# Performance work log

Hardware: AMD Instinct MI355X
Metric: run time of the kernel (lower is better)

## Reference

```python
import jax, jax.numpy as jnp
import numpy as np

ALPHA_F = 0.1
ALPHA_L = 1.0
ALPHA_E = 1.0
V_E = 10.0


def _conv3(y, w):
    # torch Conv1d(1,1,3,padding=1), cross-correlation with 3-tap kernel w
    yp = jnp.pad(y, ((0, 0), (1, 1)))  # [B, L+2]
    return w[0] * yp[:, :-2] + w[1] * yp[:, 1:-1] + w[2] * yp[:, 2:]


def setup_inputs() -> dict:
    key = jax.random.key(0)
    k1, k2 = jax.random.split(key)
    B, T, L = 32, 64, 8192
    x = jax.random.normal(k1, (B, T, L), dtype=jnp.float32)
    w = jax.random.normal(k2, (3,), dtype=jnp.float32) * 0.1  # learned Conv1d kernel
    return {"x": x, "w": w}


def reference(x, w):
    # x: [B, T, L]; PCNN recurrence over T steps
    B, T, L = x.shape
    df = jnp.asarray(np.exp(-ALPHA_F), dtype=x.dtype)
    dl = jnp.asarray(np.exp(-ALPHA_L), dtype=x.dtype)
    de = jnp.asarray(np.exp(-ALPHA_E), dtype=x.dtype)

    def step(carry, x_n):
        f, l, e, y = carry
        f = df * f + x_n + _conv3(y, w)
        # settled_weight=True: fixed kernel [1, 0, 1]
        yp = jnp.pad(y, ((0, 0), (1, 1)))
        l = dl * l + yp[:, :-2] + yp[:, 2:]
        u = f * (1.0 + 0.5 * l)
        e = de * e + V_E * y
        y = jax.nn.sigmoid(u - e)
        return (f, l, e, y), y

    z = jnp.zeros((B, L), dtype=x.dtype)
    e0 = jnp.full((B, L), V_E / ALPHA_E, dtype=x.dtype)
    _, ys = jax.lax.scan(step, (z, z, e0, z), jnp.swapaxes(x, 0, 1))  # ys: [T, B, L]
    return jnp.swapaxes(ys, 0, 1)  # [B, T, L]
```

## Files before the change

kernel.cpp:

```cpp
#include <hip/hip_runtime.h>
#include <hip/hip_bf16.h>

#define BB 32
#define TT 64
#define LL 8192
#define CC 512
#define HH 64
#define RR (CC + 2 * HH)
#define NTHREADS (RR / 2)
#define NCHUNK (LL / CC)

__device__ __forceinline__ float fsigmoid(float z) {
    float ex = __expf(-z);
    return __fdividef(1.0f, 1.0f + ex);
}

__global__ __launch_bounds__(NTHREADS) void pcnn_kernel(
    const float* __restrict__ x, const float* __restrict__ wptr,
    float* __restrict__ out)
{
    __shared__ float ylds[2 * RR];

    const int tid   = threadIdx.x;
    const int blk   = blockIdx.x;
    const int chunk = blk & (NCHUNK - 1);
    const int b     = blk >> 4;

    const float w0 = wptr[0], w1 = wptr[1], w2 = wptr[2];
    const float df = 0.90483741803595957f;
    const float dl = 0.36787944117144233f;
    const float de = 0.36787944117144233f;

    const int r0 = 2 * tid;
    const int g0 = chunk * CC - HH + r0;
    const bool valid = (g0 >= 0) && (g0 < LL);
    const bool store_en = (r0 >= HH) && (r0 < HH + CC);

    ylds[r0] = 0.0f; ylds[r0 + 1] = 0.0f;
    ylds[RR + r0] = 0.0f; ylds[RR + r0 + 1] = 0.0f;
    __syncthreads();

    float f0 = 0.f, f1 = 0.f, l0 = 0.f, l1 = 0.f;
    float e0 = 10.f, e1 = 10.f, y0 = 0.f, y1 = 0.f;

    const float* xrow = x + (size_t)b * TT * LL;
    float*       orow = out + (size_t)b * TT * LL;

    float2 xc = valid ? *(const float2*)(xrow + g0) : make_float2(0.f, 0.f);

    int cur = 0;
    for (int t = 0; t < TT; ++t) {
        float2 xn = make_float2(0.f, 0.f);
        if ((t + 1 < TT) && valid)
            xn = *(const float2*)(xrow + (size_t)(t + 1) * LL + g0);

        float yl = (r0 == 0)       ? 0.f : ylds[cur * RR + r0 - 1];
        float yr = (r0 + 2 >= RR)  ? 0.f : ylds[cur * RR + r0 + 2];

        f0 = df * f0 + xc.x + (w0 * yl + w1 * y0 + w2 * y1);
        f1 = df * f1 + xc.y + (w0 * y0 + w1 * y1 + w2 * yr);
        l0 = dl * l0 + yl + y1;
        l1 = dl * l1 + y0 + yr;
        float u0 = f0 * (1.0f + 0.5f * l0);
        float u1 = f1 * (1.0f + 0.5f * l1);
        e0 = de * e0 + 10.0f * y0;
        e1 = de * e1 + 10.0f * y1;

        float ny0 = valid ? fsigmoid(u0 - e0) : 0.f;
        float ny1 = valid ? fsigmoid(u1 - e1) : 0.f;
        y0 = ny0; y1 = ny1;

        const int nxt = cur ^ 1;
        *(float2*)&ylds[nxt * RR + r0] = make_float2(y0, y1);

        if (store_en)
            *(float2*)(orow + (size_t)t * LL + g0) = make_float2(y0, y1);

        __syncthreads();
        cur = nxt;
        xc = xn;
    }
}

extern "C" void kernel_launch(void* const* d_in, const int* in_sizes, int n_in,
                              void* d_out, int out_size, void* d_ws, size_t ws_size,
                              hipStream_t stream) {
    const float* x = (const float*)d_in[0];
    const float* w = (const float*)d_in[1];
    float* out = (float*)d_out;
    pcnn_kernel<<<dim3(BB * NCHUNK), dim3(NTHREADS), 0, stream>>>(x, w, out);
}
```

Baseline: 158.1 us.

## Map each tile to one wavefront, exchanging halos via shuffles instead of LDS barriers

Each 640-column tile (512 output plus 64-column halos) is now handled by a single 64-lane wavefront, with five float2 elements per lane held in registers. Neighbour values move through cross-lane shuffles, so the shared-memory ping-pong buffer and the per-step __syncthreads are gone. The x loads are double-buffered two time steps ahead to hide global latency. The cost is fewer threads in total (512 wavefronts in 256 blocks of 128), more registers per lane, and more serial work per lane.

```diff
diff --git a/kernel.cpp b/kernel.cpp
--- a/kernel.cpp
+++ b/kernel.cpp
@@ -1,84 +1,110 @@
 #include <hip/hip_runtime.h>
 #include <hip/hip_bf16.h>
 
-#define BB 32
+
 #define TT 64
 #define LL 8192
 #define CC 512
 #define HH 64
-#define RR (CC + 2 * HH)
-#define NTHREADS (RR / 2)
-#define NCHUNK (LL / CC)
+#define RR 640
+#define KS 5
+#define NCHUNK 16
 
 __device__ __forceinline__ float fsigmoid(float z) {
     float ex = __expf(-z);
     return __fdividef(1.0f, 1.0f + ex);
 }
 
-__global__ __launch_bounds__(NTHREADS) void pcnn_kernel(
+__global__ __launch_bounds__(128) void pcnn_wave_kernel(
     const float* __restrict__ x, const float* __restrict__ wptr,
     float* __restrict__ out)
 {
-    __shared__ float ylds[2 * RR];
-
-    const int tid   = threadIdx.x;
-    const int blk   = blockIdx.x;
-    const int chunk = blk & (NCHUNK - 1);
-    const int b     = blk >> 4;
+    const int lane = threadIdx.x & 63;
+    const int tile = blockIdx.x * 2 + (threadIdx.x >> 6);
+    const int chunk = tile & (NCHUNK - 1);
+    const int b     = tile >> 4;
 
     const float w0 = wptr[0], w1 = wptr[1], w2 = wptr[2];
     const float df = 0.90483741803595957f;
     const float dl = 0.36787944117144233f;
     const float de = 0.36787944117144233f;
 
-    const int r0 = 2 * tid;
-    const int g0 = chunk * CC - HH + r0;
-    const bool valid = (g0 >= 0) && (g0 < LL);
-    const bool store_en = (r0 >= HH) && (r0 < HH + CC);
+    const int gbase = chunk * CC - HH;
 
-    ylds[r0] = 0.0f; ylds[r0 + 1] = 0.0f;
-    ylds[RR + r0] = 0.0f; ylds[RR + r0 + 1] = 0.0f;
-    __syncthreads();
-
-    float f0 = 0.f, f1 = 0.f, l0 = 0.f, l1 = 0.f;
-    float e0 = 10.f, e1 = 10.f, y0 = 0.f, y1 = 0.f;
+    int  col[KS];
+    bool vz[KS];
+    bool st[KS];
+    #pragma unroll
+    for (int k = 0; k < KS; ++k) {
+        const int r = 128 * k + 2 * lane;
+        col[k] = gbase + r;
+        vz[k]  = (col[k] >= 0) && (col[k] < LL);
+        st[k]  = (r >= HH) && (r < HH + CC);
+    }
 
     const float* xrow = x + (size_t)b * TT * LL;
     float*       orow = out + (size_t)b * TT * LL;
 
-    float2 xc = valid ? *(const float2*)(xrow + g0) : make_float2(0.f, 0.f);
+    float2 xb[2][KS];
+    #pragma unroll
+    for (int k = 0; k < KS; ++k)
+        xb[0][k] = vz[k] ? *(const float2*)(xrow + col[k]) : make_float2(0.f, 0.f);
+    #pragma unroll
+    for (int k = 0; k < KS; ++k)
+        xb[1][k] = vz[k] ? *(const float2*)(xrow + LL + col[k]) : make_float2(0.f, 0.f);
 
-    int cur = 0;
+    float2 f[KS], l[KS], e[KS], y[KS];
+    #pragma unroll
+    for (int k = 0; k < KS; ++k) {
+        f[k] = make_float2(0.f, 0.f);
+        l[k] = make_float2(0.f, 0.f);
+        e[k] = make_float2(10.f, 10.f);
+        y[k] = make_float2(0.f, 0.f);
+    }
+
     for (int t = 0; t < TT; ++t) {
-        float2 xn = make_float2(0.f, 0.f);
-        if ((t + 1 < TT) && valid)
-            xn = *(const float2*)(xrow + (size_t)(t + 1) * LL + g0);
+        const int cur = t & 1;
+        float2 xc[KS];
+        #pragma unroll
+        for (int k = 0; k < KS; ++k) xc[k] = xb[cur][k];
 
-        float yl = (r0 == 0)       ? 0.f : ylds[cur * RR + r0 - 1];
-        float yr = (r0 + 2 >= RR)  ? 0.f : ylds[cur * RR + r0 + 2];
+        if (t + 2 < TT) {
+            const float* xnxt = xrow + (size_t)(t + 2) * LL;
+            #pragma unroll
+            for (int k = 0; k < KS; ++k)
+                xb[cur][k] = vz[k] ? *(const float2*)(xnxt + col[k]) : make_float2(0.f, 0.f);
+        }
 
-        f0 = df * f0 + xc.x + (w0 * yl + w1 * y0 + w2 * y1);
-        f1 = df * f1 + xc.y + (w0 * y0 + w1 * y1 + w2 * yr);
-        l0 = dl * l0 + yl + y1;
-        l1 = dl * l1 + y0 + yr;
-        float u0 = f0 * (1.0f + 0.5f * l0);
-        float u1 = f1 * (1.0f + 0.5f * l1);
-        e0 = de * e0 + 10.0f * y0;
-        e1 = de * e1 + 10.0f * y1;
+        float rl[KS], rr[KS], yl[KS], yr[KS];
+        #pragma unroll
+        for (int k = 0; k < KS; ++k) {
+            rl[k] = __shfl(y[k].y, (lane + 63) & 63, 64);
+            rr[k] = __shfl(y[k].x, (lane + 1) & 63, 64);
+        }
+        #pragma unroll
+        for (int k = 0; k < KS; ++k) {
+            yl[k] = (lane == 0)  ? (k > 0      ? rl[k - 1] : 0.f) : rl[k];
+            yr[k] = (lane == 63) ? (k < KS - 1 ? rr[k + 1] : 0.f) : rr[k];
+        }
 
-        float ny0 = valid ? fsigmoid(u0 - e0) : 0.f;
-        float ny1 = valid ? fsigmoid(u1 - e1) : 0.f;
-        y0 = ny0; y1 = ny1;
+        #pragma unroll
+        for (int k = 0; k < KS; ++k) {
+            f[k].x = df * f[k].x + xc[k].x + (w0 * yl[k] + w1 * y[k].x + w2 * y[k].y);
+            f[k].y = df * f[k].y + xc[k].y + (w0 * y[k].x + w1 * y[k].y + w2 * yr[k]);
+            l[k].x = dl * l[k].x + (yl[k] + y[k].y);
+            l[k].y = dl * l[k].y + (y[k].x + yr[k]);
+            const float u0 = f[k].x * (1.0f + 0.5f * l[k].x);
+            const float u1 = f[k].y * (1.0f + 0.5f * l[k].y);
+            e[k].x = de * e[k].x + 10.0f * y[k].x;
+            e[k].y = de * e[k].y + 10.0f * y[k].y;
+            y[k].x = vz[k] ? fsigmoid(u0 - e[k].x) : 0.f;
+            y[k].y = vz[k] ? fsigmoid(u1 - e[k].y) : 0.f;
+        }
 
-        const int nxt = cur ^ 1;
-        *(float2*)&ylds[nxt * RR + r0] = make_float2(y0, y1);
-
-        if (store_en)
-            *(float2*)(orow + (size_t)t * LL + g0) = make_float2(y0, y1);
-
-        __syncthreads();
-        cur = nxt;
-        xc = xn;
+        float* orowt = orow + (size_t)t * LL;
+        #pragma unroll
+        for (int k = 0; k < KS; ++k)
+            if (st[k]) *(float2*)(orowt + col[k]) = y[k];
     }
 }
 
@@ -88,5 +114,5 @@
     const float* x = (const float*)d_in[0];
     const float* w = (const float*)d_in[1];
     float* out = (float*)d_out;
-    pcnn_kernel<<<dim3(BB * NCHUNK), dim3(NTHREADS), 0, stream>>>(x, w, out);
+    pcnn_wave_kernel<<<dim3(256), dim3(128), 0, stream>>>(x, w, out);
 }
```

New measurement: 205.2 us. 29.8% more time.

## Replace block-wide LDS exchange with per-wavefront bpermute halo recurrence

Applied to the files above, without the earlier changes.

Each 64-lane wavefront now handles one 128-column tile plus a 64-column halo on each side, four values per lane. Neighbour y values are exchanged with ds_bpermute, so the per-timestep LDS writes and __syncthreads are gone. Input rows are prefetched four timesteps ahead into registers, and outputs use nontemporal stores. The cost is more redundant halo computation (half of each wavefront's work is halo) in exchange for removing block barriers.

```diff
diff --git a/kernel.cpp b/kernel.cpp
--- a/kernel.cpp
+++ b/kernel.cpp
@@ -1,84 +1,118 @@
 #include <hip/hip_runtime.h>
 #include <hip/hip_bf16.h>
 
-#define BB 32
+
 #define TT 64
 #define LL 8192
-#define CC 512
+#define CC 128
 #define HH 64
-#define RR (CC + 2 * HH)
-#define NTHREADS (RR / 2)
-#define NCHUNK (LL / CC)
+#define NCHUNK 64
 
+typedef float v2f __attribute__((ext_vector_type(2)));
+
+__device__ __forceinline__ float bperm(int idx, float v) {
+    return __int_as_float(__builtin_amdgcn_ds_bpermute(idx, __float_as_int(v)));
+}
 __device__ __forceinline__ float fsigmoid(float z) {
-    float ex = __expf(-z);
-    return __fdividef(1.0f, 1.0f + ex);
+    return __fdividef(1.0f, 1.0f + __expf(-z));
 }
 
-__global__ __launch_bounds__(NTHREADS) void pcnn_kernel(
+__global__ __launch_bounds__(256) void pcnn3_kernel(
     const float* __restrict__ x, const float* __restrict__ wptr,
     float* __restrict__ out)
 {
-    __shared__ float ylds[2 * RR];
-
-    const int tid   = threadIdx.x;
-    const int blk   = blockIdx.x;
-    const int chunk = blk & (NCHUNK - 1);
-    const int b     = blk >> 4;
+    const int lane = threadIdx.x & 63;
+    const int tile = blockIdx.x * 4 + (threadIdx.x >> 6);
+    const int chunk = tile & (NCHUNK - 1);
+    const int b     = tile >> 6;
 
     const float w0 = wptr[0], w1 = wptr[1], w2 = wptr[2];
     const float df = 0.90483741803595957f;
     const float dl = 0.36787944117144233f;
     const float de = 0.36787944117144233f;
 
-    const int r0 = 2 * tid;
-    const int g0 = chunk * CC - HH + r0;
-    const bool valid = (g0 >= 0) && (g0 < LL);
-    const bool store_en = (r0 >= HH) && (r0 < HH + CC);
+    const int r0 = 2 * lane;
+    const int c0 = chunk * CC - HH + r0;
+    const int c1 = c0 + 128;
+    const bool vz0 = ((unsigned)c0 < (unsigned)LL);
+    const bool vz1 = ((unsigned)c1 < (unsigned)LL);
+    const bool st0 = (r0 >= HH);
+    const bool st1 = (r0 < HH);
+    const int cc0 = min(max(c0, 0), LL - 2);
+    const int cc1 = min(max(c1, 0), LL - 2);
 
-    ylds[r0] = 0.0f; ylds[r0 + 1] = 0.0f;
-    ylds[RR + r0] = 0.0f; ylds[RR + r0 + 1] = 0.0f;
-    __syncthreads();
+    const float* xbase = x + (size_t)b * TT * LL;
+    const float* xp0 = xbase + cc0;
+    const float* xp1 = xbase + cc1;
+    float* op0 = out + (size_t)b * TT * LL + c0;
+    float* op1 = op0 + 128;
 
-    float f0 = 0.f, f1 = 0.f, l0 = 0.f, l1 = 0.f;
-    float e0 = 10.f, e1 = 10.f, y0 = 0.f, y1 = 0.f;
+    const int lm1 = ((lane + 63) & 63) << 2;
+    const int lp1 = ((lane + 1) & 63) << 2;
 
-    const float* xrow = x + (size_t)b * TT * LL;
-    float*       orow = out + (size_t)b * TT * LL;
+    v2f p[4][2];
+    #pragma unroll
+    for (int j = 0; j < 4; ++j) {
+        p[j][0] = *(const v2f*)(xp0 + (size_t)j * LL);
+        p[j][1] = *(const v2f*)(xp1 + (size_t)j * LL);
+    }
 
-    float2 xc = valid ? *(const float2*)(xrow + g0) : make_float2(0.f, 0.f);
+    v2f f0 = {0.f, 0.f}, f1 = {0.f, 0.f};
+    v2f l0 = {0.f, 0.f}, l1 = {0.f, 0.f};
+    v2f e0 = {10.f, 10.f}, e1 = {10.f, 10.f};
+    v2f y0 = {0.f, 0.f}, y1 = {0.f, 0.f};
 
-    int cur = 0;
-    for (int t = 0; t < TT; ++t) {
-        float2 xn = make_float2(0.f, 0.f);
-        if ((t + 1 < TT) && valid)
-            xn = *(const float2*)(xrow + (size_t)(t + 1) * LL + g0);
+    auto step = [&](v2f xa, v2f xb, float* os0, float* os1) {
+        float rl0 = bperm(lm1, y0.y), rl1 = bperm(lm1, y1.y);
+        float rr0 = bperm(lp1, y0.x), rr1 = bperm(lp1, y1.x);
+        float yl0 = (lane == 0)  ? 0.f : rl0;
+        float yl1 = (lane == 0)  ? rl0 : rl1;
+        float yr1 = (lane == 63) ? 0.f : rr1;
+        float yr0 = (lane == 63) ? rr1 : rr0;
 
-        float yl = (r0 == 0)       ? 0.f : ylds[cur * RR + r0 - 1];
-        float yr = (r0 + 2 >= RR)  ? 0.f : ylds[cur * RR + r0 + 2];
+        f0.x = df * f0.x + xa.x + (w0 * yl0  + w1 * y0.x + w2 * y0.y);
+        f0.y = df * f0.y + xa.y + (w0 * y0.x + w1 * y0.y + w2 * yr0);
+        f1.x = df * f1.x + xb.x + (w0 * yl1  + w1 * y1.x + w2 * y1.y);
+        f1.y = df * f1.y + xb.y + (w0 * y1.x + w1 * y1.y + w2 * yr1);
+        l0.x = dl * l0.x + (yl0  + y0.y);
+        l0.y = dl * l0.y + (y0.x + yr0);
+        l1.x = dl * l1.x + (yl1  + y1.y);
+        l1.y = dl * l1.y + (y1.x + yr1);
+        float u00 = f0.x * (1.0f + 0.5f * l0.x);
+        float u01 = f0.y * (1.0f + 0.5f * l0.y);
+        float u10 = f1.x * (1.0f + 0.5f * l1.x);
+        float u11 = f1.y * (1.0f + 0.5f * l1.y);
+        e0.x = de * e0.x + 10.0f * y0.x;
+        e0.y = de * e0.y + 10.0f * y0.y;
+        e1.x = de * e1.x + 10.0f * y1.x;
+        e1.y = de * e1.y + 10.0f * y1.y;
+        y0.x = vz0 ? fsigmoid(u00 - e0.x) : 0.f;
+        y0.y = vz0 ? fsigmoid(u01 - e0.y) : 0.f;
+        y1.x = vz1 ? fsigmoid(u10 - e1.x) : 0.f;
+        y1.y = vz1 ? fsigmoid(u11 - e1.y) : 0.f;
 
-        f0 = df * f0 + xc.x + (w0 * yl + w1 * y0 + w2 * y1);
-        f1 = df * f1 + xc.y + (w0 * y0 + w1 * y1 + w2 * yr);
-        l0 = dl * l0 + yl + y1;
-        l1 = dl * l1 + y0 + yr;
-        float u0 = f0 * (1.0f + 0.5f * l0);
-        float u1 = f1 * (1.0f + 0.5f * l1);
-        e0 = de * e0 + 10.0f * y0;
-        e1 = de * e1 + 10.0f * y1;
+        if (st0) __builtin_nontemporal_store(y0, (v2f*)os0);
+        if (st1) __builtin_nontemporal_store(y1, (v2f*)os1);
+    };
 
-        float ny0 = valid ? fsigmoid(u0 - e0) : 0.f;
-        float ny1 = valid ? fsigmoid(u1 - e1) : 0.f;
-        y0 = ny0; y1 = ny1;
+    const float* xl0 = xp0 + 4 * (size_t)LL;
+    const float* xl1 = xp1 + 4 * (size_t)LL;
+    float* os0 = op0;
+    float* os1 = op1;
 
-        const int nxt = cur ^ 1;
-        *(float2*)&ylds[nxt * RR + r0] = make_float2(y0, y1);
-
-        if (store_en)
-            *(float2*)(orow + (size_t)t * LL + g0) = make_float2(y0, y1);
-
-        __syncthreads();
-        cur = nxt;
-        xc = xn;
+    for (int t = 0; t < TT; t += 4) {
+        const float* a0 = (t + 8 <= TT) ? xl0 : xp0;
+        const float* a1 = (t + 8 <= TT) ? xl1 : xp1;
+        #pragma unroll
+        for (int j = 0; j < 4; ++j) {
+            step(p[j][0], p[j][1], os0, os1);
+            p[j][0] = *(const v2f*)(a0 + (size_t)j * LL);
+            p[j][1] = *(const v2f*)(a1 + (size_t)j * LL);
+            os0 += LL;
+            os1 += LL;
+        }
+        xl0 += 4 * (size_t)LL;
+        xl1 += 4 * (size_t)LL;
     }
 }
 
@@ -88,5 +122,5 @@
     const float* x = (const float*)d_in[0];
     const float* w = (const float*)d_in[1];
     float* out = (float*)d_out;
-    pcnn_kernel<<<dim3(BB * NCHUNK), dim3(NTHREADS), 0, stream>>>(x, w, out);
+    pcnn3_kernel<<<dim3(512), dim3(256), 0, stream>>>(x, w, out);
 }
```

Result: faster. 128.3 us (-18.9%).
